# Kernel tuning notes

Hardware: AMD Instinct MI355X
Metric: run time of the kernel (lower is better)

Reference implementation:

```python
import jax, jax.numpy as jnp
import numpy as np

N_NODES = 100000
N_EDGES = 1600000
IN_DIM = 48
HID = 128
BN_EPS = 1e-5


def _batchnorm(h, gamma, beta):
    # BatchNorm1d in training mode: batch mean, biased variance
    mu = jnp.mean(h, axis=0)
    var = jnp.mean(jnp.square(h - mu), axis=0)
    return (h - mu) * jax.lax.rsqrt(var + BN_EPS) * gamma + beta


def setup_inputs() -> dict:
    key = jax.random.key(0)
    ks = jax.random.split(key, 8)
    x = jax.random.normal(ks[0], (N_NODES, IN_DIM), dtype=jnp.float32)
    edge_index = jax.random.randint(ks[1], (2, N_EDGES), 0, N_NODES, dtype=jnp.int64)
    s1 = 1.0 / np.sqrt(IN_DIM)
    s2 = 1.0 / np.sqrt(HID)
    return {
        "x": x,
        "edge_index": edge_index,
        "W1": jax.random.uniform(ks[2], (HID, IN_DIM), jnp.float32, -s1, s1),
        "b1": jnp.zeros((HID,), jnp.float32),
        "g1": jnp.ones((HID,), jnp.float32),
        "be1": jnp.zeros((HID,), jnp.float32),
        "Wl": jax.random.uniform(ks[3], (HID, HID), jnp.float32, -s2, s2),
        "bl": jnp.zeros((HID,), jnp.float32),
        "Wr": jax.random.uniform(ks[4], (HID, HID), jnp.float32, -s2, s2),
        "g2": jnp.ones((HID,), jnp.float32),
        "be2": jnp.zeros((HID,), jnp.float32),
    }


def reference(x, edge_index, W1, b1, g1, be1, Wl, bl, Wr, g2, be2):
    # input projection: Linear -> BatchNorm -> ReLU
    h = x @ W1.T + b1                               # [N, HID]
    feat = jax.nn.relu(_batchnorm(h, g1, be1))      # [N, HID]

    # SAGEConv (mean aggregation): messages flow src -> dst
    src, dst = edge_index[0], edge_index[1]
    summed = jax.ops.segment_sum(feat[src], dst, num_segments=N_NODES)  # [N, HID]
    cnt = jax.ops.segment_sum(jnp.ones((N_EDGES,), jnp.float32), dst, num_segments=N_NODES)
    agg = summed / jnp.maximum(cnt, 1.0)[:, None]
    sage = agg @ Wl.T + bl + feat @ Wr.T            # lin_l(mean) + lin_r(self)

    out_feat = _batchnorm(sage, g2, be2)
    return (feat, out_feat)
```

## Files before the change

### kernel.cpp

```cpp
#include <hip/hip_runtime.h>
#include <hip/hip_bf16.h>

#define NN 100000
#define NE 1600000
#define INDIM 48
#define HID 128
#define K2 256
#define KP 64
#define BN_EPS 1e-5f

#define NBUK 391
#define BCAP 5120
#define CHUNK 8192

#define MT ((NN + 63) / 64)

typedef short s8v __attribute__((ext_vector_type(8)));
typedef float f4v __attribute__((ext_vector_type(4)));

__device__ __forceinline__ unsigned short f2bf(float f) {
    __hip_bfloat16 b = __float2bfloat16(f);
    unsigned short u;
    __builtin_memcpy(&u, &b, 2);
    return u;
}
__device__ __forceinline__ float bf2f(unsigned short u) {
    return __uint_as_float(((unsigned)u) << 16);
}

__global__ __launch_bounds__(256) void k_prep_w(const float* __restrict__ Wl, const float* __restrict__ Wr,
                                                unsigned short* __restrict__ Wcat) {
  int i = blockIdx.x * 256 + threadIdx.x;
  if (i < HID * K2) {
    int j = i >> 8, k = i & (K2 - 1);
    float v = (k < HID) ? Wl[j * HID + k] : Wr[j * HID + (k - HID)];
    Wcat[i] = f2bf(v);
  }
}

__global__ __launch_bounds__(256) void k_prep_w1(const float* __restrict__ W1,
                                                 unsigned short* __restrict__ W1b) {
  int i = blockIdx.x * 256 + threadIdx.x;
  if (i < HID * KP) {
    int j = i >> 6, k = i & (KP - 1);
    W1b[i] = (k < INDIM) ? f2bf(W1[j * INDIM + k]) : (unsigned short)0;
  }
}

__global__ __launch_bounds__(256) void k_xcast(const float* __restrict__ x,
                                               unsigned short* __restrict__ xbf) {
  int i = blockIdx.x * 256 + threadIdx.x;
  if (i >= NN * 16) return;
  int r = i >> 4, c4 = (i & 15) << 2;
  ushort4 o = {0, 0, 0, 0};
  if (c4 < INDIM) {
    float4 v = *(const float4*)(x + (size_t)r * INDIM + c4);
    o.x = f2bf(v.x);
    o.y = f2bf(v.y);
    o.z = f2bf(v.z);
    o.w = f2bf(v.w);
  }
  *(ushort4*)(xbf + (size_t)r * KP + c4) = o;
}

__global__ __launch_bounds__(256) void k_proj_gemm(
    const unsigned short* __restrict__ xbf, const unsigned short* __restrict__ W1b,
    const float* __restrict__ b1, float* __restrict__ hout,
    float* __restrict__ colSum, float* __restrict__ colSq) {
  __shared__ __align__(16) unsigned short Bsh[HID][KP + 8];
  __shared__ float redS[4][HID], redQ[4][HID];
  int tid = threadIdx.x;
  for (int i = tid; i < HID * (KP / 8); i += 256) {
    int j = i >> 3, kg = (i & 7) << 3;
    *(s8v*)&Bsh[j][kg] = *(const s8v*)(W1b + (size_t)j * KP + kg);
  }
  __syncthreads();
  int w = tid >> 6, l = tid & 63;
  int m16 = l & 15, q = l >> 4;
  float bcol[8];
#pragma unroll
  for (int nt = 0; nt < 8; ++nt) bcol[nt] = b1[nt * 16 + m16];
  float ssum[8], ssq[8];
#pragma unroll
  for (int nt = 0; nt < 8; ++nt) { ssum[nt] = 0.f; ssq[nt] = 0.f; }
  f4v zero4 = {0.f, 0.f, 0.f, 0.f};
  s8v zero8 = {0, 0, 0, 0, 0, 0, 0, 0};
  for (int tile = blockIdx.x; tile < MT; tile += gridDim.x) {
    int row = tile * 64 + w * 16 + m16;
    bool rv = row < NN;
    f4v acc[8];
#pragma unroll
    for (int nt = 0; nt < 8; ++nt) acc[nt] = zero4;
#pragma unroll
    for (int kt = 0; kt < 2; ++kt) {
      s8v a = zero8;
      if (rv) a = *(const s8v*)(xbf + (size_t)row * KP + kt * 32 + q * 8);
#pragma unroll
      for (int nt = 0; nt < 8; ++nt) {
        s8v b = *(const s8v*)(&Bsh[nt * 16 + m16][kt * 32 + q * 8]);
        acc[nt] = __builtin_amdgcn_mfma_f32_16x16x32_bf16(a, b, acc[nt], 0, 0, 0);
      }
    }
    int rbase = tile * 64 + w * 16 + q * 4;
#pragma unroll
    for (int nt = 0; nt < 8; ++nt) {
      int col = nt * 16 + m16;
#pragma unroll
      for (int r4 = 0; r4 < 4; ++r4) {
        int rr = rbase + r4;
        if (rr < NN) {
          float v = acc[nt][r4] + bcol[nt];
          hout[(size_t)rr * HID + col] = v;
          ssum[nt] += v;
          ssq[nt] = fmaf(v, v, ssq[nt]);
        }
      }
    }
  }
#pragma unroll
  for (int nt = 0; nt < 8; ++nt) {
    float s = ssum[nt], qq = ssq[nt];
    s += __shfl_xor(s, 16);
    s += __shfl_xor(s, 32);
    qq += __shfl_xor(qq, 16);
    qq += __shfl_xor(qq, 32);
    if (q == 0) {
      redS[w][nt * 16 + m16] = s;
      redQ[w][nt * 16 + m16] = qq;
    }
  }
  __syncthreads();
  if (tid < HID) {
    float s = redS[0][tid] + redS[1][tid] + redS[2][tid] + redS[3][tid];
    float qq = redQ[0][tid] + redQ[1][tid] + redQ[2][tid] + redQ[3][tid];
    atomicAdd(&colSum[tid], s);
    atomicAdd(&colSq[tid], qq);
  }
}

__global__ void k_bn_final(const float* __restrict__ sum, const float* __restrict__ sq,
                           const float* __restrict__ gamma, const float* __restrict__ beta,
                           float* __restrict__ av, float* __restrict__ bv) {
  int c = threadIdx.x;
  float mu = sum[c] * (1.0f / NN);
  float var = fmaxf(sq[c] * (1.0f / NN) - mu * mu, 0.f);
  float a = gamma[c] * rsqrtf(var + BN_EPS);
  av[c] = a;
  bv[c] = beta[c] - mu * a;
}

__global__ __launch_bounds__(256) void k_apply(float* __restrict__ feat,
                                               const float* __restrict__ av,
                                               const float* __restrict__ bv,
                                               unsigned short* __restrict__ A) {
  int i = blockIdx.x * 256 + threadIdx.x;
  if (i >= NN * 32) return;
  int r = i >> 5, c4 = (i & 31) << 2;
  float4 h = *(const float4*)(feat + (size_t)r * HID + c4);
  float4 a = *(const float4*)(av + c4);
  float4 b = *(const float4*)(bv + c4);
  float4 f;
  f.x = fmaxf(fmaf(h.x, a.x, b.x), 0.f);
  f.y = fmaxf(fmaf(h.y, a.y, b.y), 0.f);
  f.z = fmaxf(fmaf(h.z, a.z, b.z), 0.f);
  f.w = fmaxf(fmaf(h.w, a.w, b.w), 0.f);
  *(float4*)(feat + (size_t)r * HID + c4) = f;
  ushort4 o;
  o.x = f2bf(f.x);
  o.y = f2bf(f.y);
  o.z = f2bf(f.z);
  o.w = f2bf(f.w);
  *(ushort4*)(A + (size_t)r * K2 + HID + c4) = o;
}

__global__ __launch_bounds__(256) void k_bucket(const int* __restrict__ ei,
                                                int* __restrict__ bcur,
                                                unsigned int* __restrict__ bbuf) {
  __shared__ int cnt[512];
  __shared__ int sc[2][512];
  __shared__ int ofs[512];
  __shared__ int lcur[512];
  __shared__ int gbase[512];
  __shared__ unsigned int stag[CHUNK];
  __shared__ unsigned short sbkt[CHUNK];
  int tid = threadIdx.x;
  int base = blockIdx.x * CHUNK;
  int lim = min(CHUNK, NE - base);
  cnt[tid] = 0;
  cnt[tid + 256] = 0;
  __syncthreads();
#pragma unroll
  for (int i = 0; i < CHUNK / 256; ++i) {
    int e = i * 256 + tid;
    if (e < lim) {
      int d = ei[NE + base + e];
      d = min(max(d, 0), NN - 1);
      atomicAdd(&cnt[d >> 8], 1);
    }
  }
  __syncthreads();
  sc[0][tid] = cnt[tid];
  sc[0][tid + 256] = cnt[tid + 256];
  __syncthreads();
  int pp = 0;
  for (int d = 1; d < 512; d <<= 1) {
    int a0 = sc[pp][tid];
    int a1 = sc[pp][tid + 256];
    if (tid >= d) a0 += sc[pp][tid - d];
    a1 += sc[pp][tid + 256 - d];
    sc[pp ^ 1][tid] = a0;
    sc[pp ^ 1][tid + 256] = a1;
    __syncthreads();
    pp ^= 1;
  }
  ofs[tid] = sc[pp][tid] - cnt[tid];
  ofs[tid + 256] = sc[pp][tid + 256] - cnt[tid + 256];
  lcur[tid] = ofs[tid];
  lcur[tid + 256] = ofs[tid + 256];
  if (tid < NBUK) gbase[tid] = atomicAdd(&bcur[tid], cnt[tid]);
  if (tid + 256 < NBUK) gbase[tid + 256] = atomicAdd(&bcur[tid + 256], cnt[tid + 256]);
  __syncthreads();
#pragma unroll
  for (int i = 0; i < CHUNK / 256; ++i) {
    int e = i * 256 + tid;
    if (e < lim) {
      int s = ei[base + e];
      int d = ei[NE + base + e];
      s = min(max(s, 0), NN - 1);
      d = min(max(d, 0), NN - 1);
      int b = d >> 8;
      int pos = atomicAdd(&lcur[b], 1);
      stag[pos] = (unsigned)s | ((unsigned)(d & 255) << 17);
      sbkt[pos] = (unsigned short)b;
    }
  }
  __syncthreads();
  for (int s = tid; s < lim; s += 256) {
    int b = sbkt[s];
    int off = gbase[b] + (s - ofs[b]);
    if (off < BCAP) bbuf[(size_t)b * BCAP + off] = stag[s];
  }
}

__global__ __launch_bounds__(512) void k_bucket_agg(const unsigned int* __restrict__ bbuf,
                                                    const int* __restrict__ bcnt,
                                                    unsigned short* Abuf) {
  __shared__ unsigned int lcsr[BCAP];
  __shared__ int cnt[256], ofs[256], cur[256];
  __shared__ int sc[2][256];
  int tid = threadIdx.x;
  int b = blockIdx.x;
  int m = min(bcnt[b], BCAP);
  int n0 = b << 8;
  int nb = min(256, NN - n0);
  if (tid < 256) cnt[tid] = 0;
  __syncthreads();
  const unsigned int* bp = bbuf + (size_t)b * BCAP;
  for (int s = tid; s < m; s += 512) {
    unsigned p = bp[s];
    atomicAdd(&cnt[(p >> 17) & 255], 1);
  }
  __syncthreads();
  if (tid < 256) sc[0][tid] = cnt[tid];
  __syncthreads();
  int pp = 0;
  for (int d = 1; d < 256; d <<= 1) {
    if (tid < 256) {
      int v = sc[pp][tid];
      if (tid >= d) v += sc[pp][tid - d];
      sc[pp ^ 1][tid] = v;
    }
    __syncthreads();
    pp ^= 1;
  }
  if (tid < 256) {
    int o = sc[pp][tid] - cnt[tid];
    ofs[tid] = o;
    cur[tid] = o;
  }
  __syncthreads();
  for (int s = tid; s < m; s += 512) {
    unsigned p = bp[s];
    int ld = (p >> 17) & 255;
    int pos = atomicAdd(&cur[ld], 1);
    lcsr[pos] = p & 0x1FFFF;
  }
  __syncthreads();
  int lane = tid & 31;
  int g = tid >> 5;
  for (int ln = g; ln < nb; ln += 16) {
    int deg = cnt[ln], beg = ofs[ln];
    float a0 = 0.f, a1 = 0.f, a2 = 0.f, a3 = 0.f;
    int j = 0;
    for (; j + 1 < deg; j += 2) {
      int s0 = lcsr[beg + j];
      int s1 = lcsr[beg + j + 1];
      ushort4 v0 = *(const ushort4*)(Abuf + (size_t)s0 * K2 + HID + lane * 4);
      ushort4 v1 = *(const ushort4*)(Abuf + (size_t)s1 * K2 + HID + lane * 4);
      a0 += bf2f(v0.x) + bf2f(v1.x);
      a1 += bf2f(v0.y) + bf2f(v1.y);
      a2 += bf2f(v0.z) + bf2f(v1.z);
      a3 += bf2f(v0.w) + bf2f(v1.w);
    }
    if (j < deg) {
      int s0 = lcsr[beg + j];
      ushort4 v0 = *(const ushort4*)(Abuf + (size_t)s0 * K2 + HID + lane * 4);
      a0 += bf2f(v0.x);
      a1 += bf2f(v0.y);
      a2 += bf2f(v0.z);
      a3 += bf2f(v0.w);
    }
    float inv = 1.f / fmaxf((float)deg, 1.f);
    ushort4 o;
    o.x = f2bf(a0 * inv);
    o.y = f2bf(a1 * inv);
    o.z = f2bf(a2 * inv);
    o.w = f2bf(a3 * inv);
    *(ushort4*)(Abuf + (size_t)(n0 + ln) * K2 + lane * 4) = o;
  }
}

__global__ __launch_bounds__(256) void k_gemm(
    const unsigned short* __restrict__ A, const unsigned short* __restrict__ Wcat,
    const float* __restrict__ bl, float* __restrict__ sage,
    float* __restrict__ colSum, float* __restrict__ colSq) {
  __shared__ __align__(16) unsigned short Bsh[64][264];
  __shared__ float redS[4][64], redQ[4][64];
  int tid = threadIdx.x;
  int ch = blockIdx.y;
  for (int i = tid; i < 64 * 32; i += 256) {
    int j = i >> 5;
    int kg = (i & 31) << 3;
    *(s8v*)&Bsh[j][kg] = *(const s8v*)(Wcat + ((size_t)(ch * 64 + j)) * K2 + kg);
  }
  __syncthreads();
  int w = tid >> 6, l = tid & 63;
  int m16 = l & 15, q = l >> 4;
  float ssum[4] = {0.f, 0.f, 0.f, 0.f}, ssq[4] = {0.f, 0.f, 0.f, 0.f};
  f4v zero4 = {0.f, 0.f, 0.f, 0.f};
  s8v zero8 = {0, 0, 0, 0, 0, 0, 0, 0};
  for (int tile = blockIdx.x; tile < MT; tile += gridDim.x) {
    int row = tile * 64 + w * 16 + m16;
    bool rv = row < NN;
    f4v acc[4];
#pragma unroll
    for (int nt = 0; nt < 4; ++nt) acc[nt] = zero4;
#pragma unroll
    for (int kt = 0; kt < 8; ++kt) {
      s8v a = zero8;
      if (rv) a = *(const s8v*)(A + (size_t)row * K2 + kt * 32 + q * 8);
#pragma unroll
      for (int nt = 0; nt < 4; ++nt) {
        s8v bfr = *(const s8v*)(&Bsh[nt * 16 + m16][kt * 32 + q * 8]);
        acc[nt] = __builtin_amdgcn_mfma_f32_16x16x32_bf16(a, bfr, acc[nt], 0, 0, 0);
      }
    }
    int rbase = tile * 64 + w * 16 + q * 4;
#pragma unroll
    for (int nt = 0; nt < 4; ++nt) {
      int col = ch * 64 + nt * 16 + m16;
      float bv = bl[col];
#pragma unroll
      for (int r4 = 0; r4 < 4; ++r4) {
        int rr = rbase + r4;
        if (rr < NN) {
          float v = acc[nt][r4] + bv;
          sage[(size_t)rr * HID + col] = v;
          ssum[nt] += v;
          ssq[nt] = fmaf(v, v, ssq[nt]);
        }
      }
    }
  }
#pragma unroll
  for (int nt = 0; nt < 4; ++nt) {
    float s = ssum[nt], qq = ssq[nt];
    s += __shfl_xor(s, 16);
    s += __shfl_xor(s, 32);
    qq += __shfl_xor(qq, 16);
    qq += __shfl_xor(qq, 32);
    if (q == 0) {
      redS[w][nt * 16 + m16] = s;
      redQ[w][nt * 16 + m16] = qq;
    }
  }
  __syncthreads();
  if (tid < 64) {
    float s = redS[0][tid] + redS[1][tid] + redS[2][tid] + redS[3][tid];
    float qq = redQ[0][tid] + redQ[1][tid] + redQ[2][tid] + redQ[3][tid];
    atomicAdd(&colSum[ch * 64 + tid], s);
    atomicAdd(&colSq[ch * 64 + tid], qq);
  }
}

__global__ __launch_bounds__(256) void k_bn_apply(float* __restrict__ sage,
                                                  const float* __restrict__ av,
                                                  const float* __restrict__ bv) {
  int i = blockIdx.x * 256 + threadIdx.x;
  if (i < NN * HID / 4) {
    float4 s = ((const float4*)sage)[i];
    int c = (i * 4) & (HID - 1);
    float4 a = *(const float4*)(av + c);
    float4 b = *(const float4*)(bv + c);
    float4 o;
    o.x = fmaf(s.x, a.x, b.x);
    o.y = fmaf(s.y, a.y, b.y);
    o.z = fmaf(s.z, a.z, b.z);
    o.w = fmaf(s.w, a.w, b.w);
    ((float4*)sage)[i] = o;
  }
}

extern "C" void kernel_launch(void* const* d_in, const int* in_sizes, int n_in,
                              void* d_out, int out_size, void* d_ws, size_t ws_size,
                              hipStream_t stream) {
  const float* x   = (const float*)d_in[0];
  const int*   ei  = (const int*)d_in[1];
  const float* W1  = (const float*)d_in[2];
  const float* b1  = (const float*)d_in[3];
  const float* g1  = (const float*)d_in[4];
  const float* be1 = (const float*)d_in[5];
  const float* Wl  = (const float*)d_in[6];
  const float* bl  = (const float*)d_in[7];
  const float* Wr  = (const float*)d_in[8];
  const float* g2  = (const float*)d_in[9];
  const float* be2 = (const float*)d_in[10];

  float* feat_out = (float*)d_out;
  float* sage     = (float*)d_out + (size_t)NN * HID;

  size_t off = 0;
  auto alloc = [&](size_t bytes) -> void* {
    void* p = (char*)d_ws + off;
    off += (bytes + 255) & ~(size_t)255;
    return p;
  };
  unsigned short* Abuf = (unsigned short*)alloc((size_t)NN * K2 * 2);
  unsigned int*   bbuf = (unsigned int*)alloc((size_t)NBUK * BCAP * 4);
  int*            bcur = (int*)alloc((size_t)NBUK * 4);
  float*          stats = (float*)alloc(8 * HID * 4);
  float* colSum1 = stats;
  float* colSq1  = stats + HID;
  float* colSum2 = stats + 2 * HID;
  float* colSq2  = stats + 3 * HID;
  float* a1v     = stats + 4 * HID;
  float* b1v     = stats + 5 * HID;
  float* a2v     = stats + 6 * HID;
  float* b2v     = stats + 7 * HID;
  unsigned short* Wcat = (unsigned short*)alloc((size_t)HID * K2 * 2);
  unsigned short* W1b  = (unsigned short*)alloc((size_t)HID * KP * 2);
  unsigned short* xbf  = (unsigned short*)alloc((size_t)NN * KP * 2);

  hipMemsetAsync(bcur, 0, (size_t)NBUK * 4, stream);
  hipMemsetAsync(stats, 0, 4 * HID * 4, stream);

  k_prep_w<<<(HID * K2 + 255) / 256, 256, 0, stream>>>(Wl, Wr, Wcat);
  k_prep_w1<<<(HID * KP + 255) / 256, 256, 0, stream>>>(W1, W1b);
  k_xcast<<<(NN * 16 + 255) / 256, 256, 0, stream>>>(x, xbf);
  k_bucket<<<(NE + CHUNK - 1) / CHUNK, 256, 0, stream>>>(ei, bcur, bbuf);
  k_proj_gemm<<<512, 256, 0, stream>>>(xbf, W1b, b1, feat_out, colSum1, colSq1);
  k_bn_final<<<1, HID, 0, stream>>>(colSum1, colSq1, g1, be1, a1v, b1v);
  k_apply<<<(NN * 32 + 255) / 256, 256, 0, stream>>>(feat_out, a1v, b1v, Abuf);
  k_bucket_agg<<<NBUK, 512, 0, stream>>>(bbuf, bcur, Abuf);
  k_gemm<<<dim3(512, 2), 256, 0, stream>>>(Abuf, Wcat, bl, sage, colSum2, colSq2);
  k_bn_final<<<1, HID, 0, stream>>>(colSum2, colSq2, g2, be2, a2v, b2v);
  k_bn_apply<<<(NN * HID / 4 + 255) / 256, 256, 0, stream>>>(sage, a2v, b2v);
}
```

Measured before the change: 350.0 us.

## Store pre-BN projection as bf16, finer buckets, vectorized aggregation, merged prep

The projection GEMM writes pre-BN activations as bf16 directly into the aggregation buffer instead of fp32 into feat, halving that round-trip traffic before BN apply. Destination buckets shrink to 128 nodes (more blocks, smaller shared CSR), and the bucketing kernel uses 512 threads. The gather loop now loads 16 bytes per lane with two edges per warp-half and reduces with a shuffle. Memsets and weight-prep kernels are merged into a single launch. Rounding h to bf16 before BN slightly changes feat precision.

```diff
diff --git a/kernel.cpp b/kernel.cpp
--- a/kernel.cpp
+++ b/kernel.cpp
@@ -9,8 +9,8 @@
 #define KP 64
 #define BN_EPS 1e-5f
 
-#define NBUK 391
-#define BCAP 5120
+#define NBUK 782
+#define BCAP 2816
 #define CHUNK 8192
 
 #define MT ((NN + 63) / 64)
@@ -27,24 +27,32 @@
 __device__ __forceinline__ float bf2f(unsigned short u) {
     return __uint_as_float(((unsigned)u) << 16);
 }
-
-__global__ __launch_bounds__(256) void k_prep_w(const float* __restrict__ Wl, const float* __restrict__ Wr,
-                                                unsigned short* __restrict__ Wcat) {
+__device__ __forceinline__ float bflo(unsigned u) { return __uint_as_float(u << 16); }
+__device__ __forceinline__ float bfhi(unsigned u) { return __uint_as_float(u & 0xffff0000u); }
+__device__ __forceinline__ unsigned packbf(float lo, float hi) {
+    return (unsigned)f2bf(lo) | ((unsigned)f2bf(hi) << 16);
+}
+
+__global__ __launch_bounds__(256) void k_prep(const float* __restrict__ Wl, const float* __restrict__ Wr,
+                                              const float* __restrict__ W1,
+                                              unsigned short* __restrict__ Wcat,
+                                              unsigned short* __restrict__ W1b,
+                                              int* __restrict__ bcur, float* __restrict__ stats) {
   int i = blockIdx.x * 256 + threadIdx.x;
   if (i < HID * K2) {
     int j = i >> 8, k = i & (K2 - 1);
     float v = (k < HID) ? Wl[j * HID + k] : Wr[j * HID + (k - HID)];
     Wcat[i] = f2bf(v);
   }
-}
-
-__global__ __launch_bounds__(256) void k_prep_w1(const float* __restrict__ W1,
-                                                 unsigned short* __restrict__ W1b) {
-  int i = blockIdx.x * 256 + threadIdx.x;
-  if (i < HID * KP) {
-    int j = i >> 6, k = i & (KP - 1);
-    W1b[i] = (k < INDIM) ? f2bf(W1[j * INDIM + k]) : (unsigned short)0;
-  }
+  int i2 = i - HID * K2;
+  if (i2 >= 0 && i2 < HID * KP) {
+    int j = i2 >> 6, k = i2 & (KP - 1);
+    W1b[i2] = (k < INDIM) ? f2bf(W1[j * INDIM + k]) : (unsigned short)0;
+  }
+  int i3 = i2 - HID * KP;
+  if (i3 >= 0 && i3 < NBUK) bcur[i3] = 0;
+  int i4 = i3 - NBUK;
+  if (i4 >= 0 && i4 < 4 * HID) stats[i4] = 0.f;
 }
 
 __global__ __launch_bounds__(256) void k_xcast(const float* __restrict__ x,
@@ -65,7 +73,7 @@
 
 __global__ __launch_bounds__(256) void k_proj_gemm(
     const unsigned short* __restrict__ xbf, const unsigned short* __restrict__ W1b,
-    const float* __restrict__ b1, float* __restrict__ hout,
+    const float* __restrict__ b1, unsigned short* __restrict__ Abuf,
     float* __restrict__ colSum, float* __restrict__ colSq) {
   __shared__ __align__(16) unsigned short Bsh[HID][KP + 8];
   __shared__ float redS[4][HID], redQ[4][HID];
@@ -110,7 +118,7 @@
         int rr = rbase + r4;
         if (rr < NN) {
           float v = acc[nt][r4] + bcol[nt];
-          hout[(size_t)rr * HID + col] = v;
+          Abuf[(size_t)rr * K2 + HID + col] = f2bf(v);
           ssum[nt] += v;
           ssq[nt] = fmaf(v, v, ssq[nt]);
         }
@@ -154,88 +162,96 @@
                                                const float* __restrict__ bv,
                                                unsigned short* __restrict__ A) {
   int i = blockIdx.x * 256 + threadIdx.x;
-  if (i >= NN * 32) return;
-  int r = i >> 5, c4 = (i & 31) << 2;
-  float4 h = *(const float4*)(feat + (size_t)r * HID + c4);
-  float4 a = *(const float4*)(av + c4);
-  float4 b = *(const float4*)(bv + c4);
-  float4 f;
-  f.x = fmaxf(fmaf(h.x, a.x, b.x), 0.f);
-  f.y = fmaxf(fmaf(h.y, a.y, b.y), 0.f);
-  f.z = fmaxf(fmaf(h.z, a.z, b.z), 0.f);
-  f.w = fmaxf(fmaf(h.w, a.w, b.w), 0.f);
-  *(float4*)(feat + (size_t)r * HID + c4) = f;
-  ushort4 o;
-  o.x = f2bf(f.x);
-  o.y = f2bf(f.y);
-  o.z = f2bf(f.z);
-  o.w = f2bf(f.w);
-  *(ushort4*)(A + (size_t)r * K2 + HID + c4) = o;
-}
-
-__global__ __launch_bounds__(256) void k_bucket(const int* __restrict__ ei,
+  if (i >= NN * 16) return;
+  int r = i >> 4, c8 = (i & 15) << 3;
+  unsigned short* ap = A + (size_t)r * K2 + HID + c8;
+  uint4 hv = *(const uint4*)ap;
+  float4 a0 = *(const float4*)(av + c8);
+  float4 a1 = *(const float4*)(av + c8 + 4);
+  float4 b0 = *(const float4*)(bv + c8);
+  float4 b1 = *(const float4*)(bv + c8 + 4);
+  float f0 = fmaxf(fmaf(bflo(hv.x), a0.x, b0.x), 0.f);
+  float f1 = fmaxf(fmaf(bfhi(hv.x), a0.y, b0.y), 0.f);
+  float f2 = fmaxf(fmaf(bflo(hv.y), a0.z, b0.z), 0.f);
+  float f3 = fmaxf(fmaf(bfhi(hv.y), a0.w, b0.w), 0.f);
+  float f4 = fmaxf(fmaf(bflo(hv.z), a1.x, b1.x), 0.f);
+  float f5 = fmaxf(fmaf(bfhi(hv.z), a1.y, b1.y), 0.f);
+  float f6 = fmaxf(fmaf(bflo(hv.w), a1.z, b1.z), 0.f);
+  float f7 = fmaxf(fmaf(bfhi(hv.w), a1.w, b1.w), 0.f);
+  float4 o0 = {f0, f1, f2, f3}, o1 = {f4, f5, f6, f7};
+  *(float4*)(feat + (size_t)r * HID + c8) = o0;
+  *(float4*)(feat + (size_t)r * HID + c8 + 4) = o1;
+  uint4 ob;
+  ob.x = packbf(f0, f1);
+  ob.y = packbf(f2, f3);
+  ob.z = packbf(f4, f5);
+  ob.w = packbf(f6, f7);
+  *(uint4*)ap = ob;
+}
+
+__global__ __launch_bounds__(512) void k_bucket(const int* __restrict__ ei,
                                                 int* __restrict__ bcur,
                                                 unsigned int* __restrict__ bbuf) {
-  __shared__ int cnt[512];
-  __shared__ int sc[2][512];
-  __shared__ int ofs[512];
-  __shared__ int lcur[512];
-  __shared__ int gbase[512];
+  __shared__ int cnt[1024];
+  __shared__ int sc[2][1024];
+  __shared__ int ofs[1024];
+  __shared__ int lcur[1024];
+  __shared__ int gbase[1024];
   __shared__ unsigned int stag[CHUNK];
   __shared__ unsigned short sbkt[CHUNK];
   int tid = threadIdx.x;
   int base = blockIdx.x * CHUNK;
   int lim = min(CHUNK, NE - base);
   cnt[tid] = 0;
-  cnt[tid + 256] = 0;
-  __syncthreads();
-#pragma unroll
-  for (int i = 0; i < CHUNK / 256; ++i) {
-    int e = i * 256 + tid;
+  cnt[tid + 512] = 0;
+  __syncthreads();
+#pragma unroll
+  for (int i = 0; i < CHUNK / 512; ++i) {
+    int e = i * 512 + tid;
     if (e < lim) {
       int d = ei[NE + base + e];
       d = min(max(d, 0), NN - 1);
-      atomicAdd(&cnt[d >> 8], 1);
+      atomicAdd(&cnt[d >> 7], 1);
     }
   }
   __syncthreads();
   sc[0][tid] = cnt[tid];
-  sc[0][tid + 256] = cnt[tid + 256];
+  sc[0][tid + 512] = cnt[tid + 512];
   __syncthreads();
   int pp = 0;
-  for (int d = 1; d < 512; d <<= 1) {
+  for (int d = 1; d < 1024; d <<= 1) {
     int a0 = sc[pp][tid];
-    int a1 = sc[pp][tid + 256];
+    int a1 = sc[pp][tid + 512];
     if (tid >= d) a0 += sc[pp][tid - d];
-    a1 += sc[pp][tid + 256 - d];
+    a1 += sc[pp][tid + 512 - d];
     sc[pp ^ 1][tid] = a0;
-    sc[pp ^ 1][tid + 256] = a1;
+    sc[pp ^ 1][tid + 512] = a1;
     __syncthreads();
     pp ^= 1;
   }
   ofs[tid] = sc[pp][tid] - cnt[tid];
-  ofs[tid + 256] = sc[pp][tid + 256] - cnt[tid + 256];
+  ofs[tid + 512] = sc[pp][tid + 512] - cnt[tid + 512];
   lcur[tid] = ofs[tid];
-  lcur[tid + 256] = ofs[tid + 256];
+  lcur[tid + 512] = ofs[tid + 512];
   if (tid < NBUK) gbase[tid] = atomicAdd(&bcur[tid], cnt[tid]);
-  if (tid + 256 < NBUK) gbase[tid + 256] = atomicAdd(&bcur[tid + 256], cnt[tid + 256]);
-  __syncthreads();
-#pragma unroll
-  for (int i = 0; i < CHUNK / 256; ++i) {
-    int e = i * 256 + tid;
+  if (tid + 512 < NBUK) gbase[tid + 512] = atomicAdd(&bcur[tid + 512], cnt[tid + 512]);
+  __syncthreads();
+#pragma unroll
+  for (int i = 0; i < CHUNK / 512; ++i) {
+    int e = i * 512 + tid;
     if (e < lim) {
       int s = ei[base + e];
       int d = ei[NE + base + e];
       s = min(max(s, 0), NN - 1);
       d = min(max(d, 0), NN - 1);
-      int b = d >> 8;
+      int b = d >> 7;
       int pos = atomicAdd(&lcur[b], 1);
-      stag[pos] = (unsigned)s | ((unsigned)(d & 255) << 17);
+      stag[pos] = (unsigned)s | ((unsigned)(d & 127) << 17);
       sbkt[pos] = (unsigned short)b;
     }
   }
   __syncthreads();
-  for (int s = tid; s < lim; s += 256) {
+  for (int s = tid; s < lim; s += 512) {
     int b = sbkt[s];
     int off = gbase[b] + (s - ofs[b]);
     if (off < BCAP) bbuf[(size_t)b * BCAP + off] = stag[s];
@@ -246,26 +262,26 @@
                                                     const int* __restrict__ bcnt,
                                                     unsigned short* Abuf) {
   __shared__ unsigned int lcsr[BCAP];
-  __shared__ int cnt[256], ofs[256], cur[256];
-  __shared__ int sc[2][256];
+  __shared__ int cnt[128], ofs[128], cur[128];
+  __shared__ int sc[2][128];
   int tid = threadIdx.x;
   int b = blockIdx.x;
   int m = min(bcnt[b], BCAP);
-  int n0 = b << 8;
-  int nb = min(256, NN - n0);
-  if (tid < 256) cnt[tid] = 0;
+  int n0 = b << 7;
+  int nb = min(128, NN - n0);
+  if (tid < 128) cnt[tid] = 0;
   __syncthreads();
   const unsigned int* bp = bbuf + (size_t)b * BCAP;
   for (int s = tid; s < m; s += 512) {
     unsigned p = bp[s];
-    atomicAdd(&cnt[(p >> 17) & 255], 1);
-  }
-  __syncthreads();
-  if (tid < 256) sc[0][tid] = cnt[tid];
+    atomicAdd(&cnt[(p >> 17) & 127], 1);
+  }
+  __syncthreads();
+  if (tid < 128) sc[0][tid] = cnt[tid];
   __syncthreads();
   int pp = 0;
-  for (int d = 1; d < 256; d <<= 1) {
-    if (tid < 256) {
+  for (int d = 1; d < 128; d <<= 1) {
+    if (tid < 128) {
       int v = sc[pp][tid];
       if (tid >= d) v += sc[pp][tid - d];
       sc[pp ^ 1][tid] = v;
@@ -273,7 +289,7 @@
     __syncthreads();
     pp ^= 1;
   }
-  if (tid < 256) {
+  if (tid < 128) {
     int o = sc[pp][tid] - cnt[tid];
     ofs[tid] = o;
     cur[tid] = o;
@@ -281,42 +297,47 @@
   __syncthreads();
   for (int s = tid; s < m; s += 512) {
     unsigned p = bp[s];
-    int ld = (p >> 17) & 255;
+    int ld = (p >> 17) & 127;
     int pos = atomicAdd(&cur[ld], 1);
     lcsr[pos] = p & 0x1FFFF;
   }
   __syncthreads();
   int lane = tid & 31;
   int g = tid >> 5;
+  int half = lane >> 4;
+  int l16 = lane & 15;
   for (int ln = g; ln < nb; ln += 16) {
     int deg = cnt[ln], beg = ofs[ln];
-    float a0 = 0.f, a1 = 0.f, a2 = 0.f, a3 = 0.f;
+    float aL[4] = {0.f, 0.f, 0.f, 0.f}, aH[4] = {0.f, 0.f, 0.f, 0.f};
     int j = 0;
-    for (; j + 1 < deg; j += 2) {
-      int s0 = lcsr[beg + j];
-      int s1 = lcsr[beg + j + 1];
-      ushort4 v0 = *(const ushort4*)(Abuf + (size_t)s0 * K2 + HID + lane * 4);
-      ushort4 v1 = *(const ushort4*)(Abuf + (size_t)s1 * K2 + HID + lane * 4);
-      a0 += bf2f(v0.x) + bf2f(v1.x);
-      a1 += bf2f(v0.y) + bf2f(v1.y);
-      a2 += bf2f(v0.z) + bf2f(v1.z);
-      a3 += bf2f(v0.w) + bf2f(v1.w);
-    }
-    if (j < deg) {
-      int s0 = lcsr[beg + j];
-      ushort4 v0 = *(const ushort4*)(Abuf + (size_t)s0 * K2 + HID + lane * 4);
-      a0 += bf2f(v0.x);
-      a1 += bf2f(v0.y);
-      a2 += bf2f(v0.z);
-      a3 += bf2f(v0.w);
+#pragma unroll 2
+    for (; j + 2 <= deg; j += 2) {
+      int s = lcsr[beg + j + half];
+      uint4 v = *(const uint4*)(Abuf + (size_t)s * K2 + HID + l16 * 8);
+      aL[0] += bflo(v.x); aH[0] += bfhi(v.x);
+      aL[1] += bflo(v.y); aH[1] += bfhi(v.y);
+      aL[2] += bflo(v.z); aH[2] += bfhi(v.z);
+      aL[3] += bflo(v.w); aH[3] += bfhi(v.w);
+    }
+    if (j < deg && half == 0) {
+      int s = lcsr[beg + j];
+      uint4 v = *(const uint4*)(Abuf + (size_t)s * K2 + HID + l16 * 8);
+      aL[0] += bflo(v.x); aH[0] += bfhi(v.x);
+      aL[1] += bflo(v.y); aH[1] += bfhi(v.y);
+      aL[2] += bflo(v.z); aH[2] += bfhi(v.z);
+      aL[3] += bflo(v.w); aH[3] += bfhi(v.w);
     }
     float inv = 1.f / fmaxf((float)deg, 1.f);
-    ushort4 o;
-    o.x = f2bf(a0 * inv);
-    o.y = f2bf(a1 * inv);
-    o.z = f2bf(a2 * inv);
-    o.w = f2bf(a3 * inv);
-    *(ushort4*)(Abuf + (size_t)(n0 + ln) * K2 + lane * 4) = o;
+    uint4 o;
+    unsigned* op = &o.x;
+#pragma unroll
+    for (int i = 0; i < 4; ++i) {
+      float lo = aL[i] + __shfl_xor(aL[i], 16);
+      float hi = aH[i] + __shfl_xor(aH[i], 16);
+      op[i] = packbf(lo * inv, hi * inv);
+    }
+    if (half == 0)
+      *(uint4*)(Abuf + (size_t)(n0 + ln) * K2 + l16 * 8) = o;
   }
 }
 
@@ -451,16 +472,13 @@
   unsigned short* W1b  = (unsigned short*)alloc((size_t)HID * KP * 2);
   unsigned short* xbf  = (unsigned short*)alloc((size_t)NN * KP * 2);
 
-  hipMemsetAsync(bcur, 0, (size_t)NBUK * 4, stream);
-  hipMemsetAsync(stats, 0, 4 * HID * 4, stream);
-
-  k_prep_w<<<(HID * K2 + 255) / 256, 256, 0, stream>>>(Wl, Wr, Wcat);
-  k_prep_w1<<<(HID * KP + 255) / 256, 256, 0, stream>>>(W1, W1b);
+  int prep_n = HID * K2 + HID * KP + NBUK + 4 * HID;
+  k_prep<<<(prep_n + 255) / 256, 256, 0, stream>>>(Wl, Wr, W1, Wcat, W1b, bcur, stats);
   k_xcast<<<(NN * 16 + 255) / 256, 256, 0, stream>>>(x, xbf);
-  k_bucket<<<(NE + CHUNK - 1) / CHUNK, 256, 0, stream>>>(ei, bcur, bbuf);
-  k_proj_gemm<<<512, 256, 0, stream>>>(xbf, W1b, b1, feat_out, colSum1, colSq1);
+  k_bucket<<<(NE + CHUNK - 1) / CHUNK, 512, 0, stream>>>(ei, bcur, bbuf);
+  k_proj_gemm<<<512, 256, 0, stream>>>(xbf, W1b, b1, Abuf, colSum1, colSq1);
   k_bn_final<<<1, HID, 0, stream>>>(colSum1, colSq1, g1, be1, a1v, b1v);
-  k_apply<<<(NN * 32 + 255) / 256, 256, 0, stream>>>(feat_out, a1v, b1v, Abuf);
+  k_apply<<<(NN * 16 + 255) / 256, 256, 0, stream>>>(feat_out, a1v, b1v, Abuf);
   k_bucket_agg<<<NBUK, 512, 0, stream>>>(bbuf, bcur, Abuf);
   k_gemm<<<dim3(512, 2), 256, 0, stream>>>(Abuf, Wcat, bl, sage, colSum2, colSq2);
   k_bn_final<<<1, HID, 0, stream>>>(colSum2, colSq2, g2, be2, a2v, b2v);
```

Measured after the change: 326.4 us. 6.7% less time.
